# Kernel tuning notes

Hardware: AMD Instinct MI355X
Metric: run time of the kernel (lower is better)

Reference implementation:

```python
import jax, jax.numpy as jnp
import numpy as np

H, DQK, DV, DM, POS = 8, 64, 64, 768, 64

def _rel_basis(l, n):
    # Enformer central-mask relative position basis: [l, l, n]
    pos = jnp.arange(l)
    distance = pos[None, :] - pos[:, None]              # [l, l] int
    half = n // 2
    pow_rate = jnp.exp(jnp.log(jnp.asarray((l + 1) / 2.0, jnp.float32)) / half)
    center_widths = pow_rate ** jnp.arange(1, half + 1, dtype=jnp.float32)  # [half]
    unsigned = (jnp.abs(distance)[:, :, None].astype(jnp.float32) <= center_widths)
    signed = jnp.sign(distance)[:, :, None] * unsigned
    return jnp.concatenate([unsigned.astype(jnp.float32), signed.astype(jnp.float32)], axis=-1)

def setup_inputs() -> dict:
    key = jax.random.key(0)
    ks = jax.random.split(key, 9)
    b, l = 2, 1024
    x = jax.random.normal(ks[0], (b, l, DM), jnp.float32)
    # torch Linear weights: [out, in]
    Wq = jax.random.normal(ks[1], (H * DQK, DM), jnp.float32) * (1.0 / np.sqrt(DM))
    Wk = jax.random.normal(ks[2], (H * DQK, DM), jnp.float32) * (1.0 / np.sqrt(DM))
    Wv = jax.random.normal(ks[3], (H * DV, DM), jnp.float32) * (1.0 / np.sqrt(DM))
    Wo = jax.random.normal(ks[4], (DM, H * DV), jnp.float32) * (1.0 / np.sqrt(H * DV))
    bo = jnp.zeros((DM,), jnp.float32)
    u_bias = jax.random.normal(ks[5], (H, DQK), jnp.float32) * np.sqrt(2.0 / DQK)
    v_bias = jax.random.normal(ks[6], (H, DQK), jnp.float32) * np.sqrt(2.0 / DQK)
    w_pos = jax.random.normal(ks[7], (H, DQK, POS), jnp.float32) * np.sqrt(2.0 / POS)
    return {"x": x, "Wq": Wq, "Wk": Wk, "Wv": Wv, "Wo": Wo, "bo": bo,
            "u_bias": u_bias, "v_bias": v_bias, "w_pos": w_pos}

def reference(x, Wq, Wk, Wv, Wo, bo, u_bias, v_bias, w_pos):
    b, l, _ = x.shape
    q = (x @ Wq.T).reshape(b, l, H, DQK)
    k = (x @ Wk.T).reshape(b, l, H, DQK)
    v = (x @ Wv.T).reshape(b, l, H, DV)
    basis = _rel_basis(l, POS)                           # [l, l, n]
    scale = 1.0 / np.sqrt(DQK)
    # qr_term: einsum('bihd,hdn,ijn->bhij') factored to avoid [b,h,l,l,d]
    qw = jnp.einsum('bihd,hdn->bhin', q, w_pos)          # [b,h,l,n]
    qr = jnp.einsum('bhin,ijn->bhij', qw, basis)
    uk = jnp.einsum('hd,bjhd->bhj', u_bias, k)[:, :, None, :]
    vw = jnp.einsum('hd,hdn->hn', v_bias, w_pos)
    vr = jnp.einsum('hn,ijn->hij', vw, basis)[None]      # [1,h,l,l]
    bias = (qr + uk + vr) * scale
    scores = jnp.einsum('bihd,bjhd->bhij', q, k) * scale + bias
    attn = jax.nn.softmax(scores, axis=-1)
    out = jnp.einsum('bhij,bjhd->bihd', attn, v).reshape(b, l, H * DV)
    return out @ Wo.T + bo
```

## Files before the change

kernel.cpp:

```cpp
#include <hip/hip_runtime.h>

#define LSEQ 1024
#define NB   2
#define NH   8
#define DD   64
#define DMOD 768

using bf16x8 = __attribute__((ext_vector_type(8))) short;
using f32x4  = __attribute__((ext_vector_type(4))) float;

__device__ inline unsigned short f2bf(float f) {
    union { float f; unsigned u; } v; v.f = f;
    unsigned r = v.u + 0x7FFFu + ((v.u >> 16) & 1u);
    return (unsigned short)(r >> 16);
}

__global__ __launch_bounds__(256) void pack_setup(
    const float4* __restrict__ x,  const float4* __restrict__ wq,
    const float4* __restrict__ wk, const float4* __restrict__ wv,
    const float4* __restrict__ wo,
    const float* __restrict__ u_bias, const float* __restrict__ v_bias,
    const float* __restrict__ w_pos,
    ushort4* __restrict__ xb, ushort4* __restrict__ wqb, ushort4* __restrict__ wkb,
    ushort4* __restrict__ wvb, ushort4* __restrict__ wob,
    float* __restrict__ wsfx, unsigned char* __restrict__ cls_g)
{
    int tid = threadIdx.x;
    if (blockIdx.x >= 3072) {
        int sb = blockIdx.x - 3072;
        if (sb == 0) {
            __shared__ float w_s[32];
            __shared__ int cmin_s[1024];
            if (tid < 32) {
                float pr = expf(logf(512.5f) / 32.0f);
                w_s[tid] = powf(pr, (float)(tid + 1));
            }
            __syncthreads();
            for (int d = tid; d < 1024; d += 256) {
                float fd = (float)d;
                int cm = 32;
                for (int c = 31; c >= 0; --c) if (fd <= w_s[c]) cm = c;
                cmin_s[d] = cm;
            }
            __syncthreads();
            for (int d2 = tid; d2 < 2048; d2 += 256) {
                int dd = d2 - 1023;
                int ad = dd < 0 ? -dd : dd; if (ad > 1023) ad = 1023;
                int t = (dd < 0) ? 0 : ((dd == 0) ? 1 : 2);
                cls_g[d2] = (unsigned char)(t * 33 + cmin_s[ad]);
            }
        } else {
            int h = sb - 1;
            __shared__ float vred[4][64];
            __shared__ float ured[4][64];
            __shared__ float wd[64];
            int n = tid & 63, g = tid >> 6;
            float vs = 0.f, us = 0.f;
#pragma unroll
            for (int k = 0; k < 16; ++k) {
                int d = g * 16 + k;
                float wp = w_pos[(h * 64 + d) * 64 + n];
                vs += v_bias[h * 64 + d] * wp;
                us += u_bias[h * 64 + d] * wp;
            }
            vred[g][n] = vs; ured[g][n] = us;
            __syncthreads();
            if (tid < 64) {
                float v4 = vred[0][tid] + vred[1][tid] + vred[2][tid] + vred[3][tid];
                float u4 = ured[0][tid] + ured[1][tid] + ured[2][tid] + ured[3][tid];
                wd[tid] = v4 - u4;
            }
            __syncthreads();
            if (tid < 64) {
                int nn = tid & 31, cb = tid & 32;
                float s = 0.f;
                for (int c = 31; c >= nn; --c) s += wd[cb + c];
                wsfx[h * 64 + tid] = s * 0.125f;
            }
        }
        return;
    }
    int i = blockIdx.x * 256 + tid;
    const float4* src; ushort4* dst; int off;
    if (i < 393216)      { src = x;  dst = xb;  off = i; }
    else if (i < 491520) { src = wq; dst = wqb; off = i - 393216; }
    else if (i < 589824) { src = wk; dst = wkb; off = i - 491520; }
    else if (i < 688128) { src = wv; dst = wvb; off = i - 589824; }
    else                 { src = wo; dst = wob; off = i - 688128; }
    float4 v = src[off];
    ushort4 o;
    o.x = f2bf(v.x); o.y = f2bf(v.y); o.z = f2bf(v.z); o.w = f2bf(v.w);
    dst[off] = o;
}

__global__ __launch_bounds__(256) void gemm_qkv(
    const unsigned short* __restrict__ X, const unsigned short* __restrict__ W,
    const float* __restrict__ ub,
    unsigned short* __restrict__ Qb, unsigned short* __restrict__ Kb,
    unsigned short* __restrict__ Vtb)
{
    __shared__ unsigned short Xs[64][40];
    __shared__ unsigned short Wsm[64][40];
    __shared__ unsigned short Ct[64][72];

    int tid = threadIdx.x;
    int w = tid >> 6, lane = tid & 63, l15 = lane & 15, q = lane >> 4;
    int M0 = blockIdx.y * 64, N0 = blockIdx.x * 64;
    int rs = tid >> 2, seg = tid & 3;

    f32x4 acc[4] = {};
    for (int k0 = 0; k0 < 768; k0 += 32) {
        uint4 xv = *(const uint4*)(X + (size_t)(M0 + rs) * 768 + k0 + seg * 8);
        uint4 wv = *(const uint4*)(W + (size_t)(N0 + rs) * 768 + k0 + seg * 8);
        *(uint4*)&Xs[rs][seg * 8]  = xv;
        *(uint4*)&Wsm[rs][seg * 8] = wv;
        __syncthreads();
        bf16x8 a = *(bf16x8*)&Xs[w * 16 + l15][q * 8];
#pragma unroll
        for (int ct = 0; ct < 4; ++ct) {
            bf16x8 bfr = *(bf16x8*)&Wsm[ct * 16 + l15][q * 8];
            acc[ct] = __builtin_amdgcn_mfma_f32_16x16x32_bf16(a, bfr, acc[ct], 0, 0, 0);
        }
        __syncthreads();
    }

    if (N0 < 1024) {
        int isQ = (N0 < 512);
#pragma unroll
        for (int ct = 0; ct < 4; ++ct) {
            float u0 = isQ ? ub[N0 + ct * 16 + l15] : 0.f;
            float sc = isQ ? 0.125f : 1.0f;
#pragma unroll
            for (int r = 0; r < 4; ++r)
                Ct[w * 16 + q * 4 + r][ct * 16 + l15] = f2bf((acc[ct][r] + u0) * sc);
        }
        __syncthreads();
        int Nh = isQ ? N0 : (N0 - 512);
        unsigned short* out = isQ ? Qb : Kb;
        size_t base = ((size_t)((M0 >> 10) * 8 + (Nh >> 6)) * 1024 + (M0 & 1023)) * 64;
#pragma unroll
        for (int it = 0; it < 2; ++it) {
            int idx = tid + it * 256;
            int row = idx >> 3, sg = idx & 7;
            *(uint4*)(out + base + (size_t)row * 64 + sg * 8) = *(uint4*)&Ct[row][sg * 8];
        }
    } else {
#pragma unroll
        for (int ct = 0; ct < 4; ++ct) {
            ushort4 pk;
            pk.x = f2bf(acc[ct][0]); pk.y = f2bf(acc[ct][1]);
            pk.z = f2bf(acc[ct][2]); pk.w = f2bf(acc[ct][3]);
            *(ushort4*)&Ct[ct * 16 + l15][w * 16 + q * 4] = pk;
        }
        __syncthreads();
        size_t base = ((size_t)((M0 >> 10) * 8 + ((N0 - 1024) >> 6))) * 65536;
        int j0 = M0 & 1023;
#pragma unroll
        for (int it = 0; it < 2; ++it) {
            int idx = tid + it * 256;
            int d = idx >> 3, sg = idx & 7;
            *(uint4*)(Vtb + base + (size_t)d * 1024 + j0 + sg * 8) = *(uint4*)&Ct[d][sg * 8];
        }
    }
}

__global__ __launch_bounds__(256) void gemm_o(
    const unsigned short* __restrict__ X, const unsigned short* __restrict__ W,
    const float* __restrict__ bias, float* __restrict__ out)
{
    __shared__ unsigned short Xs[64][40];
    __shared__ unsigned short Wsm[64][40];
    __shared__ float Ctf[64][72];

    int tid = threadIdx.x;
    int w = tid >> 6, lane = tid & 63, l15 = lane & 15, q = lane >> 4;
    int M0 = blockIdx.y * 64, N0 = blockIdx.x * 64;
    int rs = tid >> 2, seg = tid & 3;

    f32x4 acc[4] = {};
    for (int k0 = 0; k0 < 512; k0 += 32) {
        uint4 xv = *(const uint4*)(X + (size_t)(M0 + rs) * 512 + k0 + seg * 8);
        uint4 wv = *(const uint4*)(W + (size_t)(N0 + rs) * 512 + k0 + seg * 8);
        *(uint4*)&Xs[rs][seg * 8]  = xv;
        *(uint4*)&Wsm[rs][seg * 8] = wv;
        __syncthreads();
        bf16x8 a = *(bf16x8*)&Xs[w * 16 + l15][q * 8];
#pragma unroll
        for (int ct = 0; ct < 4; ++ct) {
            bf16x8 bfr = *(bf16x8*)&Wsm[ct * 16 + l15][q * 8];
            acc[ct] = __builtin_amdgcn_mfma_f32_16x16x32_bf16(a, bfr, acc[ct], 0, 0, 0);
        }
        __syncthreads();
    }
#pragma unroll
    for (int ct = 0; ct < 4; ++ct) {
        float bv = bias[N0 + ct * 16 + l15];
#pragma unroll
        for (int r = 0; r < 4; ++r)
            Ctf[w * 16 + q * 4 + r][ct * 16 + l15] = acc[ct][r] + bv;
    }
    __syncthreads();
#pragma unroll
    for (int it = 0; it < 4; ++it) {
        int idx = tid + it * 256;
        int row = idx >> 4, sg = idx & 15;
        *(float4*)(out + (size_t)(M0 + row) * 768 + N0 + sg * 4) = *(float4*)&Ctf[row][sg * 4];
    }
}

__global__ __launch_bounds__(256, 4) void attn_mfma(
    const unsigned short* __restrict__ Qbf,
    const unsigned short* __restrict__ Kbf,
    const unsigned short* __restrict__ Vt,
    const float* __restrict__ w_pos,
    const float* __restrict__ wsfx,
    const unsigned char* __restrict__ cls_g,
    unsigned short* __restrict__ ao)
{
    __shared__ float biasT[16 * 99];
    __shared__ unsigned char cls[2048];
    __shared__ unsigned short Pl[4][16][76];
    union Ovl {
        struct { unsigned short wptS[64][68]; float qwL[16][68]; } pre;
        struct { float Obuf[4][64][17]; float lbuf[4][16]; } post;
    };
    __shared__ Ovl ovl;

    int tid = threadIdx.x;
    int b = blockIdx.z, h = blockIdx.y, bh = b * 8 + h;
    int i0 = blockIdx.x * 16;
    int w = tid >> 6, lane = tid & 63, l15 = lane & 15, q = lane >> 4;

    for (int idx = tid; idx < 512; idx += 256)
        ((unsigned int*)cls)[idx] = ((const unsigned int*)cls_g)[idx];
    {
        const float4* wsrc = (const float4*)(w_pos + h * 4096);
#pragma unroll
        for (int it = 0; it < 4; ++it) {
            int f = tid + it * 256;
            float4 wv = wsrc[f];
            int d = f >> 4, n4 = (f & 15) * 4;
            ovl.pre.wptS[n4 + 0][d] = f2bf(wv.x);
            ovl.pre.wptS[n4 + 1][d] = f2bf(wv.y);
            ovl.pre.wptS[n4 + 2][d] = f2bf(wv.z);
            ovl.pre.wptS[n4 + 3][d] = f2bf(wv.w);
        }
    }

    int ig = i0 + l15;
    const unsigned short* qrow = Qbf + ((size_t)bh * 1024 + ig) * 64;
    bf16x8 qf0 = *(const bf16x8*)(qrow + q * 8);
    bf16x8 qf1 = *(const bf16x8*)(qrow + 32 + q * 8);
    __syncthreads();

    {
        bf16x8 b0 = *(bf16x8*)&ovl.pre.wptS[w * 16 + l15][q * 8];
        bf16x8 b1 = *(bf16x8*)&ovl.pre.wptS[w * 16 + l15][32 + q * 8];
        f32x4 a = {};
        a = __builtin_amdgcn_mfma_f32_16x16x32_bf16(qf0, b0, a, 0, 0, 0);
        a = __builtin_amdgcn_mfma_f32_16x16x32_bf16(qf1, b1, a, 0, 0, 0);
#pragma unroll
        for (int r = 0; r < 4; ++r)
            ovl.pre.qwL[q * 4 + r][w * 16 + l15] = a[r];
    }
    __syncthreads();

    const float* wsh = wsfx + h * 64;
#pragma unroll
    for (int it = 0; it < 4; ++it) {
        int idx = tid + it * 256;
        int il = idx >> 6, n = idx & 63, nn = n & 31, cb = n & 32;
        float run = 0.f, s = 0.f;
#pragma unroll
        for (int c = 31; c >= 0; --c) {
            run += ovl.pre.qwL[il][cb + c];
            if (c == nn) s = run;
        }
        ovl.pre.qwL[il][n] = s + wsh[n];
    }
    __syncthreads();

    for (int idx = tid; idx < 528; idx += 256) {
        int il = idx / 33, c = idx - il * 33;
        float up = 0.f, sp = 0.f;
        if (c < 32) {
            up = ovl.pre.qwL[il][c];
            sp = ovl.pre.qwL[il][32 + c];
        }
        float* bt = biasT + il * 99;
        bt[c]      = up - sp;
        bt[33 + c] = up;
        bt[66 + c] = up + sp;
    }
    __syncthreads();

    const unsigned short* Kbase = Kbf + (size_t)bh * 65536;
    const unsigned short* Vbase = Vt  + (size_t)bh * 65536;
    const float* btrow = biasT + l15 * 99;
    int clsoff = 1023 - ig;

    f32x4 Oacc[4] = {};
    float lsum = 0.f;

    for (int jt = 0; jt < 4; ++jt) {
        int jb = w * 256 + jt * 64;
        f32x4 st[4];
#pragma unroll
        for (int ct = 0; ct < 4; ++ct) {
            const unsigned short* krow = Kbase + (size_t)(jb + ct * 16 + l15) * 64;
            bf16x8 ka0 = *(const bf16x8*)(krow + q * 8);
            bf16x8 ka1 = *(const bf16x8*)(krow + 32 + q * 8);
            f32x4 a = {};
            a = __builtin_amdgcn_mfma_f32_16x16x32_bf16(ka0, qf0, a, 0, 0, 0);
            a = __builtin_amdgcn_mfma_f32_16x16x32_bf16(ka1, qf1, a, 0, 0, 0);
            st[ct] = a;
        }
#pragma unroll
        for (int ct = 0; ct < 4; ++ct) {
            int d2b = jb + ct * 16 + q * 4 + clsoff;
            float pv[4];
#pragma unroll
            for (int r = 0; r < 4; ++r) {
                float s = st[ct][r] + btrow[cls[d2b + r]];
                float p = __expf(s);
                lsum += p;
                pv[r] = p;
            }
            ushort4 pk;
            pk.x = f2bf(pv[0]); pk.y = f2bf(pv[1]);
            pk.z = f2bf(pv[2]); pk.w = f2bf(pv[3]);
            *(ushort4*)&Pl[w][l15][ct * 16 + q * 4] = pk;
        }
#pragma unroll
        for (int ks = 0; ks < 2; ++ks) {
            bf16x8 pb = *(const bf16x8*)&Pl[w][l15][ks * 32 + q * 8];
#pragma unroll
            for (int dt = 0; dt < 4; ++dt) {
                bf16x8 va = *(const bf16x8*)(Vbase + (size_t)(dt * 16 + l15) * 1024
                                             + jb + ks * 32 + q * 8);
                Oacc[dt] = __builtin_amdgcn_mfma_f32_16x16x32_bf16(va, pb, Oacc[dt], 0, 0, 0);
            }
        }
    }

    lsum += __shfl_xor(lsum, 16);
    lsum += __shfl_xor(lsum, 32);

    __syncthreads();
#pragma unroll
    for (int dt = 0; dt < 4; ++dt)
#pragma unroll
        for (int r = 0; r < 4; ++r)
            ovl.post.Obuf[w][dt * 16 + q * 4 + r][l15] = Oacc[dt][r];
    if (lane < 16) ovl.post.lbuf[w][l15] = lsum;
    __syncthreads();

    for (int t2 = tid; t2 < 1024; t2 += 256) {
        int il = t2 >> 6, d = t2 & 63;
        float o = ovl.post.Obuf[0][d][il] + ovl.post.Obuf[1][d][il]
                + ovl.post.Obuf[2][d][il] + ovl.post.Obuf[3][d][il];
        float l = ovl.post.lbuf[0][il] + ovl.post.lbuf[1][il]
                + ovl.post.lbuf[2][il] + ovl.post.lbuf[3][il];
        ao[((size_t)(b * 1024 + i0 + il)) * 512 + h * 64 + d] = f2bf(o / l);
    }
}

extern "C" void kernel_launch(void* const* d_in, const int* in_sizes, int n_in,
                              void* d_out, int out_size, void* d_ws, size_t ws_size,
                              hipStream_t stream)
{
    const float* x      = (const float*)d_in[0];
    const float* Wq     = (const float*)d_in[1];
    const float* Wk     = (const float*)d_in[2];
    const float* Wv     = (const float*)d_in[3];
    const float* Wo     = (const float*)d_in[4];
    const float* bo     = (const float*)d_in[5];
    const float* u_bias = (const float*)d_in[6];
    const float* v_bias = (const float*)d_in[7];
    const float* w_pos  = (const float*)d_in[8];
    float* out = (float*)d_out;

    char* ws = (char*)d_ws;
    unsigned short* Xbf  = (unsigned short*)ws;            ws += 3145728;
    unsigned short* Wqkv = (unsigned short*)ws;            ws += 2359296;
    unsigned short* Wob  = (unsigned short*)ws;            ws += 786432;
    unsigned short* Qbf  = (unsigned short*)ws;            ws += 2097152;
    unsigned short* Kbf  = (unsigned short*)ws;            ws += 2097152;
    unsigned short* Vtb  = (unsigned short*)ws;            ws += 2097152;
    unsigned short* aob  = (unsigned short*)ws;            ws += 2097152;
    float*          wsfx = (float*)ws;                     ws += 2048;
    unsigned char*  clsg = (unsigned char*)ws;             ws += 2048;

    pack_setup<<<3081, 256, 0, stream>>>(
        (const float4*)x, (const float4*)Wq, (const float4*)Wk,
        (const float4*)Wv, (const float4*)Wo,
        u_bias, v_bias, w_pos,
        (ushort4*)Xbf,
        (ushort4*)Wqkv, (ushort4*)Wqkv + 98304, (ushort4*)Wqkv + 196608,
        (ushort4*)Wob,
        wsfx, clsg);

    gemm_qkv<<<dim3(24, 32), 256, 0, stream>>>(Xbf, Wqkv, u_bias, Qbf, Kbf, Vtb);

    attn_mfma<<<dim3(64, 8, 2), 256, 0, stream>>>(
        Qbf, Kbf, Vtb, w_pos, wsfx, clsg, aob);

    gemm_o<<<dim3(12, 32), 256, 0, stream>>>(aob, Wob, bo, out);
}
```

Baseline: 137.0 us.

## Fuse fp32-to-bf16 packing into GEMM loads and drop separate pack kernel

Removes the standalone pack_setup kernel that converted x and all weights to bf16 in workspace. The QKV and output GEMMs now load fp32 tiles directly and convert to bf16 in registers before staging to shared memory. The small setup work (relative-position class table and per-head suffix sums) moves into an extra grid row of the QKV GEMM. This saves a launch plus a full write and re-read of the bf16 copies, but each GEMM tile now reads twice the bytes from global memory and does the conversion redundantly across blocks that share tiles.

```diff
diff --git a/kernel.cpp b/kernel.cpp
--- a/kernel.cpp
+++ b/kernel.cpp
@@ -1,4 +1,5 @@
 #include <hip/hip_runtime.h>
+#include <hip/hip_bf16.h>
 
 #define LSEQ 1024
 #define NB   2
@@ -14,20 +15,26 @@
     unsigned r = v.u + 0x7FFFu + ((v.u >> 16) & 1u);
     return (unsigned short)(r >> 16);
 }
-
-__global__ __launch_bounds__(256) void pack_setup(
-    const float4* __restrict__ x,  const float4* __restrict__ wq,
-    const float4* __restrict__ wk, const float4* __restrict__ wv,
-    const float4* __restrict__ wo,
+__device__ inline unsigned pk2bf(float a, float b) {
+    union { __hip_bfloat162 h; unsigned u; } c;
+    c.h = __float22bfloat162_rn(make_float2(a, b));
+    return c.u;
+}
+
+__global__ __launch_bounds__(256) void gemm_qkv(
+    const float* __restrict__ X,
+    const float* __restrict__ Wq, const float* __restrict__ Wk,
+    const float* __restrict__ Wv,
     const float* __restrict__ u_bias, const float* __restrict__ v_bias,
     const float* __restrict__ w_pos,
-    ushort4* __restrict__ xb, ushort4* __restrict__ wqb, ushort4* __restrict__ wkb,
-    ushort4* __restrict__ wvb, ushort4* __restrict__ wob,
+    unsigned short* __restrict__ Qb, unsigned short* __restrict__ Kb,
+    unsigned short* __restrict__ Vtb,
     float* __restrict__ wsfx, unsigned char* __restrict__ cls_g)
 {
     int tid = threadIdx.x;
-    if (blockIdx.x >= 3072) {
-        int sb = blockIdx.x - 3072;
+
+    if (blockIdx.y == 32) {
+        int sb = blockIdx.x;
         if (sb == 0) {
             __shared__ float w_s[32];
             __shared__ int cmin_s[1024];
@@ -49,7 +56,7 @@
                 int t = (dd < 0) ? 0 : ((dd == 0) ? 1 : 2);
                 cls_g[d2] = (unsigned char)(t * 33 + cmin_s[ad]);
             }
-        } else {
+        } else if (sb <= 8) {
             int h = sb - 1;
             __shared__ float vred[4][64];
             __shared__ float ured[4][64];
@@ -80,40 +87,36 @@
         }
         return;
     }
-    int i = blockIdx.x * 256 + tid;
-    const float4* src; ushort4* dst; int off;
-    if (i < 393216)      { src = x;  dst = xb;  off = i; }
-    else if (i < 491520) { src = wq; dst = wqb; off = i - 393216; }
-    else if (i < 589824) { src = wk; dst = wkb; off = i - 491520; }
-    else if (i < 688128) { src = wv; dst = wvb; off = i - 589824; }
-    else                 { src = wo; dst = wob; off = i - 688128; }
-    float4 v = src[off];
-    ushort4 o;
-    o.x = f2bf(v.x); o.y = f2bf(v.y); o.z = f2bf(v.z); o.w = f2bf(v.w);
-    dst[off] = o;
-}
-
-__global__ __launch_bounds__(256) void gemm_qkv(
-    const unsigned short* __restrict__ X, const unsigned short* __restrict__ W,
-    const float* __restrict__ ub,
-    unsigned short* __restrict__ Qb, unsigned short* __restrict__ Kb,
-    unsigned short* __restrict__ Vtb)
-{
+
     __shared__ unsigned short Xs[64][40];
     __shared__ unsigned short Wsm[64][40];
     __shared__ unsigned short Ct[64][72];
 
-    int tid = threadIdx.x;
     int w = tid >> 6, lane = tid & 63, l15 = lane & 15, q = lane >> 4;
     int M0 = blockIdx.y * 64, N0 = blockIdx.x * 64;
     int rs = tid >> 2, seg = tid & 3;
 
+    const float* Wsrc; int Nrow;
+    if (N0 < 512)       { Wsrc = Wq; Nrow = N0; }
+    else if (N0 < 1024) { Wsrc = Wk; Nrow = N0 - 512; }
+    else                { Wsrc = Wv; Nrow = N0 - 1024; }
+
+    const float* xrow = X    + (size_t)(M0 + rs) * 768 + seg * 8;
+    const float* wrow = Wsrc + (size_t)(Nrow + rs) * 768 + seg * 8;
+
     f32x4 acc[4] = {};
     for (int k0 = 0; k0 < 768; k0 += 32) {
-        uint4 xv = *(const uint4*)(X + (size_t)(M0 + rs) * 768 + k0 + seg * 8);
-        uint4 wv = *(const uint4*)(W + (size_t)(N0 + rs) * 768 + k0 + seg * 8);
-        *(uint4*)&Xs[rs][seg * 8]  = xv;
-        *(uint4*)&Wsm[rs][seg * 8] = wv;
+        float4 xa = *(const float4*)(xrow + k0);
+        float4 xb = *(const float4*)(xrow + k0 + 4);
+        float4 wa = *(const float4*)(wrow + k0);
+        float4 wb = *(const float4*)(wrow + k0 + 4);
+        uint4 xp, wp;
+        xp.x = pk2bf(xa.x, xa.y); xp.y = pk2bf(xa.z, xa.w);
+        xp.z = pk2bf(xb.x, xb.y); xp.w = pk2bf(xb.z, xb.w);
+        wp.x = pk2bf(wa.x, wa.y); wp.y = pk2bf(wa.z, wa.w);
+        wp.z = pk2bf(wb.x, wb.y); wp.w = pk2bf(wb.z, wb.w);
+        *(uint4*)&Xs[rs][seg * 8]  = xp;
+        *(uint4*)&Wsm[rs][seg * 8] = wp;
         __syncthreads();
         bf16x8 a = *(bf16x8*)&Xs[w * 16 + l15][q * 8];
 #pragma unroll
@@ -128,7 +131,7 @@
         int isQ = (N0 < 512);
 #pragma unroll
         for (int ct = 0; ct < 4; ++ct) {
-            float u0 = isQ ? ub[N0 + ct * 16 + l15] : 0.f;
+            float u0 = isQ ? u_bias[N0 + ct * 16 + l15] : 0.f;
             float sc = isQ ? 0.125f : 1.0f;
 #pragma unroll
             for (int r = 0; r < 4; ++r)
@@ -165,7 +168,7 @@
 }
 
 __global__ __launch_bounds__(256) void gemm_o(
-    const unsigned short* __restrict__ X, const unsigned short* __restrict__ W,
+    const unsigned short* __restrict__ X, const float* __restrict__ W,
     const float* __restrict__ bias, float* __restrict__ out)
 {
     __shared__ unsigned short Xs[64][40];
@@ -177,12 +180,18 @@
     int M0 = blockIdx.y * 64, N0 = blockIdx.x * 64;
     int rs = tid >> 2, seg = tid & 3;
 
+    const float* wrow = W + (size_t)(N0 + rs) * 512 + seg * 8;
+
     f32x4 acc[4] = {};
     for (int k0 = 0; k0 < 512; k0 += 32) {
         uint4 xv = *(const uint4*)(X + (size_t)(M0 + rs) * 512 + k0 + seg * 8);
-        uint4 wv = *(const uint4*)(W + (size_t)(N0 + rs) * 512 + k0 + seg * 8);
+        float4 wa = *(const float4*)(wrow + k0);
+        float4 wb = *(const float4*)(wrow + k0 + 4);
+        uint4 wp;
+        wp.x = pk2bf(wa.x, wa.y); wp.y = pk2bf(wa.z, wa.w);
+        wp.z = pk2bf(wb.x, wb.y); wp.w = pk2bf(wb.z, wb.w);
         *(uint4*)&Xs[rs][seg * 8]  = xv;
-        *(uint4*)&Wsm[rs][seg * 8] = wv;
+        *(uint4*)&Wsm[rs][seg * 8] = wp;
         __syncthreads();
         bf16x8 a = *(bf16x8*)&Xs[w * 16 + l15][q * 8];
 #pragma unroll
@@ -381,9 +390,6 @@
     float* out = (float*)d_out;
 
     char* ws = (char*)d_ws;
-    unsigned short* Xbf  = (unsigned short*)ws;            ws += 3145728;
-    unsigned short* Wqkv = (unsigned short*)ws;            ws += 2359296;
-    unsigned short* Wob  = (unsigned short*)ws;            ws += 786432;
     unsigned short* Qbf  = (unsigned short*)ws;            ws += 2097152;
     unsigned short* Kbf  = (unsigned short*)ws;            ws += 2097152;
     unsigned short* Vtb  = (unsigned short*)ws;            ws += 2097152;
@@ -391,19 +397,12 @@
     float*          wsfx = (float*)ws;                     ws += 2048;
     unsigned char*  clsg = (unsigned char*)ws;             ws += 2048;
 
-    pack_setup<<<3081, 256, 0, stream>>>(
-        (const float4*)x, (const float4*)Wq, (const float4*)Wk,
-        (const float4*)Wv, (const float4*)Wo,
-        u_bias, v_bias, w_pos,
-        (ushort4*)Xbf,
-        (ushort4*)Wqkv, (ushort4*)Wqkv + 98304, (ushort4*)Wqkv + 196608,
-        (ushort4*)Wob,
-        wsfx, clsg);
-
-    gemm_qkv<<<dim3(24, 32), 256, 0, stream>>>(Xbf, Wqkv, u_bias, Qbf, Kbf, Vtb);
+    gemm_qkv<<<dim3(24, 33), 256, 0, stream>>>(
+        x, Wq, Wk, Wv, u_bias, v_bias, w_pos,
+        Qbf, Kbf, Vtb, wsfx, clsg);
 
     attn_mfma<<<dim3(64, 8, 2), 256, 0, stream>>>(
         Qbf, Kbf, Vtb, w_pos, wsfx, clsg, aob);
 
-    gemm_o<<<dim3(12, 32), 256, 0, stream>>>(aob, Wob, bo, out);
-}
+    gemm_o<<<dim3(12, 32), 256, 0, stream>>>(aob, Wo, bo, out);
+}
```

Measured after the change: 138.8 us. About the same (+1.3%).
